# Performance work log

Measured on AMD Instinct MI355X. Metric: run time of the kernel, lower is better.

Reference implementation:

```python
import jax, jax.numpy as jnp
import numpy as np

NUM_GROUPS = 32
EPS = 1e-6


def setup_inputs() -> dict:
    key = jax.random.key(0)
    ks = jax.random.split(key, 10)
    B, C, L = 8, 512, 4096
    s = 1.0 / np.sqrt(C)
    x = jax.random.normal(ks[0], (B, C, L), dtype=jnp.float32)
    gn_w = jnp.ones((C,), jnp.float32)
    gn_b = jnp.zeros((C,), jnp.float32)
    wq = jax.random.normal(ks[1], (C, C), jnp.float32) * s
    bq = jax.random.normal(ks[2], (C,), jnp.float32) * 0.01
    wk = jax.random.normal(ks[3], (C, C), jnp.float32) * s
    bk = jax.random.normal(ks[4], (C,), jnp.float32) * 0.01
    wv = jax.random.normal(ks[5], (C, C), jnp.float32) * s
    bv = jax.random.normal(ks[6], (C,), jnp.float32) * 0.01
    wo = jax.random.normal(ks[7], (C, C), jnp.float32) * s
    bo = jax.random.normal(ks[8], (C,), jnp.float32) * 0.01
    return {"x": x, "gn_w": gn_w, "gn_b": gn_b, "wq": wq, "bq": bq,
            "wk": wk, "bk": bk, "wv": wv, "bv": bv, "wo": wo, "bo": bo}


def _group_norm(x, w, b):
    # x: [B, C, L]; normalize over each group's (C/G, L) slice
    B, C, L = x.shape
    g = x.reshape(B, NUM_GROUPS, C // NUM_GROUPS, L)
    mu = jnp.mean(g, axis=(2, 3), keepdims=True)
    var = jnp.var(g, axis=(2, 3), keepdims=True)
    g = (g - mu) * jax.lax.rsqrt(var + EPS)
    return g.reshape(B, C, L) * w[None, :, None] + b[None, :, None]


def _conv1x1(h, w, b):
    # pointwise conv: [B,C,L] x [Cout,Cin] -> [B,Cout,L]
    return jnp.einsum('oc,bcl->bol', w, h) + b[None, :, None]


def reference(x, gn_w, gn_b, wq, bq, wk, bk, wv, bv, wo, bo):
    h = _group_norm(x, gn_w, gn_b)
    q = _conv1x1(h, wq, bq)
    k = _conv1x1(h, wk, bk)
    v = _conv1x1(h, wv, bv)
    B, C, L = q.shape
    scale = jnp.asarray(C, q.dtype) ** -0.5
    # w_[b,i,j] = sum_c q[b,c,i] k[b,c,j]
    w_ = jnp.einsum('bci,bcj->bij', q, k) * scale
    w_ = jax.nn.softmax(w_, axis=2)
    # h[b,c,i] = sum_j v[b,c,j] w_[b,i,j]
    h = jnp.einsum('bcj,bij->bci', v, w_)
    return x + _conv1x1(h, wo, bo)
```

## Files before the change

kernel.cpp:

```cpp
#include <hip/hip_runtime.h>
#include <hip/hip_bf16.h>
#include <math.h>

#define DI __device__ __forceinline__

typedef unsigned short u16;
typedef unsigned int   u32;
typedef unsigned long long u64;
typedef __attribute__((ext_vector_type(8))) short short8;
typedef __attribute__((ext_vector_type(4))) float f32x4;

constexpr int CB = 512;
constexpr int LL = 4096;
constexpr int NG = 32;
constexpr long NELC = (long)LL * CB;

DI float bf2f(u16 u) { u32 v = ((u32)u) << 16; float f; __builtin_memcpy(&f, &v, 4); return f; }
DI u16 f2bf(float f) {
  u32 u; __builtin_memcpy(&u, &f, 4);
  u += 0x7fffu + ((u >> 16) & 1u);
  return (u16)(u >> 16);
}

DI void gload16(const void* g, void* l) {
  __builtin_amdgcn_global_load_lds((const __attribute__((address_space(1))) u32*)g,
                                   (__attribute__((address_space(3))) u32*)l, 16, 0, 0);
}

__global__ __launch_bounds__(256) void prep(
    const float* __restrict__ wq, const float* __restrict__ wk,
    const float* __restrict__ wv, const float* __restrict__ wo,
    const float* __restrict__ bq, const float* __restrict__ bk,
    const float* __restrict__ bv, const float* __restrict__ x,
    u16* __restrict__ wqkv, u16* __restrict__ wob, float* __restrict__ bqkv,
    float* __restrict__ stats) {
  if (blockIdx.x < 1024) {
    int i = blockIdx.x * 256 + threadIdx.x;
    wqkv[i]          = f2bf(wq[i]);
    wqkv[262144 + i] = f2bf(wk[i]);
    wqkv[524288 + i] = f2bf(wv[i]);
    wob[i]           = f2bf(wo[i]);
  } else if (blockIdx.x == 1024) {
    for (int j = 0; j < 6; ++j) {
      int idx = j * 256 + threadIdx.x;
      float b = (idx < 512) ? bq[idx] : (idx < 1024) ? bk[idx - 512] : bv[idx - 1024];
      bqkv[idx] = b;
    }
  } else {
    const int bid = blockIdx.x - 1025;
    const float4* base = (const float4*)(x + (long)bid * (16 * LL));
    float s = 0.f, ss = 0.f;
    for (int i = threadIdx.x; i < 16 * LL / 4; i += 256) {
      float4 v = base[i];
      s  += v.x + v.y + v.z + v.w;
      ss += v.x * v.x + v.y * v.y + v.z * v.z + v.w * v.w;
    }
#pragma unroll
    for (int o = 32; o; o >>= 1) { s += __shfl_xor(s, o); ss += __shfl_xor(ss, o); }
    __shared__ float red[8];
    int wv2 = threadIdx.x >> 6, ln = threadIdx.x & 63;
    if (ln == 0) { red[wv2 * 2] = s; red[wv2 * 2 + 1] = ss; }
    __syncthreads();
    if (threadIdx.x == 0) {
      float S = red[0] + red[2] + red[4] + red[6];
      float SS = red[1] + red[3] + red[5] + red[7];
      float mu = S * (1.f / 65536.f);
      float var = SS * (1.f / 65536.f) - mu * mu;
      stats[bid * 2]     = mu;
      stats[bid * 2 + 1] = rsqrtf(var + 1e-6f);
    }
  }
}

__global__ __launch_bounds__(256) void gn_apply(
    const float* __restrict__ x, const float* __restrict__ gw,
    const float* __restrict__ gb, const float* __restrict__ stats,
    u16* __restrict__ hT) {
  __shared__ u16 t[64][66];
  const int b = blockIdx.z, c0 = blockIdx.y * 64, l0 = blockIdx.x * 64;
  const int tid = threadIdx.x;
#pragma unroll
  for (int p = 0; p < 4; ++p) {
    const int cr = p * 16 + (tid >> 4);
    const int lq = (tid & 15) * 4;
    const int c = c0 + cr;
    const float mu = stats[(b * NG + (c >> 4)) * 2];
    const float rs = stats[(b * NG + (c >> 4)) * 2 + 1];
    const float g = gw[c], be = gb[c];
    float4 v = *(const float4*)(x + (long)b * CB * LL + (long)c * LL + l0 + lq);
    t[cr][lq + 0] = f2bf((v.x - mu) * rs * g + be);
    t[cr][lq + 1] = f2bf((v.y - mu) * rs * g + be);
    t[cr][lq + 2] = f2bf((v.z - mu) * rs * g + be);
    t[cr][lq + 3] = f2bf((v.w - mu) * rs * g + be);
  }
  __syncthreads();
#pragma unroll
  for (int it = 0; it < 2; ++it) {
    const int i = it * 2048 + tid * 8;
    const int lr = i >> 6, cc = i & 63;
    short8 val;
#pragma unroll
    for (int j = 0; j < 8; ++j) val[j] = (short)t[cc + j][lr];
    *(short8*)(hT + (long)b * LL * CB + (long)(l0 + lr) * CB + c0 + cc) = val;
  }
}

template <int Q>
DI void rdA(const u16* LB, int wr, int fr, int fq, short8 af[2][2]) {
#pragma unroll
  for (int m2 = 0; m2 < 2; ++m2)
#pragma unroll
    for (int kk = 0; kk < 2; ++kk) {
      const int R = wr * 128 + (Q * 2 + m2) * 16 + fr;
      af[m2][kk] = *(const short8*)((const char*)LB + R * 128 +
                                    ((kk * 64 + fq * 16) ^ ((R & 7) << 4)));
    }
}
DI void rdB(const u16* LB, int wc, int fr, int fq, short8 bf[4][2]) {
#pragma unroll
  for (int nf = 0; nf < 4; ++nf)
#pragma unroll
    for (int kk = 0; kk < 2; ++kk) {
      const int R = wc * 64 + nf * 16 + fr;
      bf[nf][kk] = *(const short8*)((const char*)LB + R * 128 +
                                    ((kk * 64 + fq * 16) ^ ((R & 7) << 4)));
    }
}
template <int Q>
DI void mmaQ(short8 af[2][2], short8 bf[4][2], f32x4 acc[8][4]) {
#pragma unroll
  for (int kk = 0; kk < 2; ++kk)
#pragma unroll
    for (int m2 = 0; m2 < 2; ++m2)
#pragma unroll
      for (int nf = 0; nf < 4; ++nf)
        acc[Q * 2 + m2][nf] = __builtin_amdgcn_mfma_f32_16x16x32_bf16(
            af[m2][kk], bf[nf][kk], acc[Q * 2 + m2][nf], 0, 0, 0);
}

#define PTAIL(Q)                                             \
  __builtin_amdgcn_s_barrier();                              \
  asm volatile("s_waitcnt lgkmcnt(0)" ::: "memory");         \
  __builtin_amdgcn_sched_barrier(0);                         \
  __builtin_amdgcn_s_setprio(1);                             \
  mmaQ<Q>(af, bf, acc);                                      \
  __builtin_amdgcn_s_setprio(0);                             \
  __builtin_amdgcn_s_barrier();

template <int EPI>
__global__ __launch_bounds__(512, 2) void gemm8p(
    const u16* __restrict__ A, int lda, long asb,
    const u16* __restrict__ Bt, int ldb, long bsb,
    int K, const float* __restrict__ bias, float scale,
    u16* __restrict__ o0, u16* __restrict__ o1, u16* __restrict__ o2,
    const float* __restrict__ rls, float* __restrict__ spp,
    long osb, int ldo) {
  __shared__ u16 smem[65536];
  u16* lA0 = smem;
  u16* lA1 = smem + 16384;
  u16* lB0 = smem + 32768;
  u16* lB1 = smem + 49152;

  const int tid = threadIdx.x;
  const int lane = tid & 63, wv = tid >> 6;
  const int wr = wv >> 2, wc = wv & 3;
  const int fr = lane & 15, fq = lane >> 4;
  const int bx = blockIdx.x, by = blockIdx.y, bz = blockIdx.z;
  const int bzb = (EPI == 2) ? (bz >> 2) : bz;
  const int tb  = (EPI == 2) ? (bz & 3) * (K >> 6) : 0;

  const u16* Ab = A + (long)bzb * asb + (long)(by * 256) * lda;
  const u16* Bb = Bt + (long)bzb * bsb + (long)(bx * 256) * ldb;

  auto stage = [&](u16* lbase, const u16* gbase, int ld_, int half, int t) {
#pragma unroll
    for (int p = 0; p < 2; ++p) {
      int i = p * 512 + tid;
      int row = i >> 3, ch = i & 7;
      int src = t * 64 + ((((ch << 4) ^ ((row & 7) << 4))) >> 1);
      gload16(gbase + (long)(half * 128 + row) * ld_ + src,
              lbase + half * 8192 + i * 8);
    }
  };

  f32x4 acc[8][4];
#pragma unroll
  for (int m = 0; m < 8; ++m)
#pragma unroll
    for (int n = 0; n < 4; ++n) acc[m][n] = (f32x4)(0.f);

  stage(lA0, Ab, lda, 0, tb); stage(lA0, Ab, lda, 1, tb);
  stage(lB0, Bb, ldb, 0, tb); stage(lB0, Bb, ldb, 1, tb);
  stage(lB1, Bb, ldb, 0, tb + 1); stage(lB1, Bb, ldb, 1, tb + 1);
  asm volatile("s_waitcnt vmcnt(4)" ::: "memory");
  __builtin_amdgcn_sched_barrier(0);
  __builtin_amdgcn_s_barrier();

  const int nt = K >> 6;
  short8 af[2][2], bf[4][2];
  for (int i = 0; i < nt / 2; ++i) {
    const bool last = (i == nt / 2 - 1);
    const int t1 = tb + 2 * i + 1, t2 = tb + 2 * i + 2, t3 = tb + 2 * i + 3;
    rdB(lB0, wc, fr, fq, bf);
    rdA<0>(lA0, wr, fr, fq, af);
    stage(lA1, Ab, lda, 0, t1);
    PTAIL(0)
    rdA<1>(lA0, wr, fr, fq, af);
    stage(lA1, Ab, lda, 1, t1);
    PTAIL(1)
    rdA<2>(lA0, wr, fr, fq, af);
    if (!last) stage(lB0, Bb, ldb, 0, t2);
    PTAIL(2)
    rdA<3>(lA0, wr, fr, fq, af);
    if (!last) stage(lB0, Bb, ldb, 1, t2);
    if (last) { asm volatile("s_waitcnt vmcnt(0)" ::: "memory"); }
    else      { asm volatile("s_waitcnt vmcnt(4)" ::: "memory"); }
    __builtin_amdgcn_sched_barrier(0);
    PTAIL(3)
    rdB(lB1, wc, fr, fq, bf);
    rdA<0>(lA1, wr, fr, fq, af);
    if (!last) stage(lA0, Ab, lda, 0, t2);
    PTAIL(0)
    rdA<1>(lA1, wr, fr, fq, af);
    if (!last) stage(lA0, Ab, lda, 1, t2);
    PTAIL(1)
    rdA<2>(lA1, wr, fr, fq, af);
    if (!last) stage(lB1, Bb, ldb, 0, t3);
    PTAIL(2)
    rdA<3>(lA1, wr, fr, fq, af);
    if (!last) stage(lB1, Bb, ldb, 1, t3);
    if (!last) {
      asm volatile("s_waitcnt vmcnt(4)" ::: "memory");
      __builtin_amdgcn_sched_barrier(0);
    }
    PTAIL(3)
  }

  if constexpr (EPI == 1) {
#pragma unroll
    for (int mf = 0; mf < 8; ++mf)
#pragma unroll
      for (int nf = 0; nf < 4; ++nf) {
        const int nl = wc * 64 + nf * 16 + fr;
#pragma unroll
        for (int r = 0; r < 4; ++r) {
          const int ml = wr * 128 + mf * 16 + fq * 4 + r;
          smem[ml * 256 + (nl ^ ((ml & 7) << 3))] =
              f2bf(exp2f(acc[mf][nf][r] * scale));
        }
      }
    __syncthreads();
    u16* dst0 = o0 + (long)bz * osb + (long)(by * 256) * ldo + bx * 256;
    float* sppb = spp + ((long)bz * 16 + bx) * LL + by * 256;
    for (int i = tid * 8; i < 65536; i += 4096) {
      const int rr = i >> 8, cc = i & 255;
      short8 val = *(const short8*)&smem[rr * 256 + (cc ^ ((rr & 7) << 3))];
      *(short8*)(dst0 + (long)rr * ldo + cc) = val;
      float s = 0.f;
#pragma unroll
      for (int j = 0; j < 8; ++j) s += bf2f((u16)val[j]);
      s += __shfl_xor(s, 1);  s += __shfl_xor(s, 2);
      s += __shfl_xor(s, 4);  s += __shfl_xor(s, 8);
      s += __shfl_xor(s, 16);
      if ((tid & 31) == 0) sppb[rr] = s;
    }
  } else if constexpr (EPI == 2) {
    const float* rl = rls + (long)bzb * LL + by * 256;
#pragma unroll
    for (int mf = 0; mf < 8; ++mf)
#pragma unroll
      for (int nf = 0; nf < 4; ++nf) {
        const int nl = wc * 64 + nf * 16 + fr;
#pragma unroll
        for (int r = 0; r < 4; ++r) {
          const int ml = wr * 128 + mf * 16 + fq * 4 + r;
          smem[ml * 256 + (nl ^ ((ml & 7) << 3))] =
              f2bf(acc[mf][nf][r] * rl[ml]);
        }
      }
    __syncthreads();
    u16* dst0 = o0 + (long)bzb * 4 * NELC + (long)(by * 256) * 2048 +
                (bz & 3) * 512 + bx * 256;
    for (int i = tid * 8; i < 65536; i += 4096) {
      const int rr = i >> 8, cc = i & 255;
      short8 val = *(const short8*)&smem[rr * 256 + (cc ^ ((rr & 7) << 3))];
      *(short8*)(dst0 + (long)rr * 2048 + cc) = val;
    }
  } else {
    const int mat = by >> 1;
    if (mat < 2) {
#pragma unroll
      for (int mf = 0; mf < 8; ++mf)
#pragma unroll
        for (int nf = 0; nf < 4; ++nf) {
          const int nl = wc * 64 + nf * 16 + fr;
#pragma unroll
          for (int r = 0; r < 4; ++r) {
            const int ml = wr * 128 + mf * 16 + fq * 4 + r;
            smem[nl * 256 + (ml ^ ((nl & 7) << 3))] =
                f2bf(acc[mf][nf][r] + bias[by * 256 + ml]);
          }
        }
      __syncthreads();
      u16* dst0 = (mat == 0 ? o0 : o1) + (long)bz * NELC +
                  (long)(bx * 256) * CB + ((by * 256) & 511);
      for (int i = tid * 8; i < 65536; i += 4096) {
        const int rr = i >> 8, cc = i & 255;
        short8 val = *(const short8*)&smem[rr * 256 + (cc ^ ((rr & 7) << 3))];
        *(short8*)(dst0 + (long)rr * CB + cc) = val;
      }
    } else {
#pragma unroll
      for (int mf = 0; mf < 8; ++mf)
#pragma unroll
        for (int nf = 0; nf < 4; ++nf) {
          const int nl = wc * 64 + nf * 16 + fr;
#pragma unroll
          for (int r = 0; r < 4; ++r) {
            const int ml = wr * 128 + mf * 16 + fq * 4 + r;
            smem[ml * 256 + (nl ^ ((ml & 7) << 3))] =
                f2bf(acc[mf][nf][r] + bias[by * 256 + ml]);
          }
        }
      __syncthreads();
      u16* dst0 = o2 + (long)bz * ((long)CB * LL) +
                  (long)((by * 256) & 511) * LL + bx * 256;
      for (int i = tid * 8; i < 65536; i += 4096) {
        const int rr = i >> 8, cc = i & 255;
        short8 val = *(const short8*)&smem[rr * 256 + (cc ^ ((rr & 7) << 3))];
        *(short8*)(dst0 + (long)rr * LL + cc) = val;
      }
    }
  }
}

template <int BM, int BN, int EPI, bool SWZ, int WR, int WC>
__global__ __launch_bounds__(WR * WC * 64) void gemm_bt(
    const u16* __restrict__ A, int lda, long asb,
    const u16* __restrict__ Bt, int ldb, long bsb,
    int K, const float* __restrict__ bias, float scale,
    u16* __restrict__ o0, u16* __restrict__ o1, u16* __restrict__ o2,
    float* __restrict__ of, const float* __restrict__ xres, long osb, int ldo) {
  constexpr int NT = WR * WC * 64;
  constexpr int FM = BM / WR / 16, FN = BN / WC / 16;
  static_assert((BM * 8) % NT == 0 && (BN * 8) % NT == 0, "staging div");
  __shared__ u16 smem[(BM + BN) * 64];
  u16* lA = smem;
  u16* lB = smem + BM * 64;

  int bx = blockIdx.x, by = blockIdx.y;
  if constexpr (SWZ) {
    const int nwg = gridDim.x * gridDim.y;
    const int id = by * gridDim.x + bx;
    const int id2 = (id & 7) * (nwg >> 3) + (id >> 3);
    bx = id2 % gridDim.x;
    by = id2 / gridDim.x;
  }

  const int tid = threadIdx.x;
  const int lane = tid & 63;
  const int wv = tid >> 6;
  const int wr = wv / WC, wc = wv % WC;
  const int fr = lane & 15, fq = lane >> 4;
  const int bz = blockIdx.z;
  const int bzb  = (EPI == 4) ? (bz >> 1) : bz;
  const int kbeg = (EPI == 4) ? (bz & 1) * K : 0;

  const u16* Ab = A + (long)bzb * asb + (long)(by * BM) * lda;
  const u16* Bb = Bt + (long)bzb * bsb + (long)(bx * BN) * ldb;

  f32x4 acc[FM][FN];
#pragma unroll
  for (int m = 0; m < FM; ++m)
#pragma unroll
    for (int n = 0; n < FN; ++n) acc[m][n] = (f32x4)(0.f);

  for (int k0 = kbeg; k0 < kbeg + K; k0 += 64) {
#pragma unroll
    for (int p = 0; p < BM * 8 / NT; ++p) {
      int t = p * NT + tid;
      int row = t >> 3;
      int cbl = ((t & 7) << 4) ^ ((row & 7) << 4);
      gload16(Ab + (long)row * lda + k0 + (cbl >> 1), &lA[t * 8]);
    }
#pragma unroll
    for (int p = 0; p < BN * 8 / NT; ++p) {
      int t = p * NT + tid;
      int row = t >> 3;
      int cbl = ((t & 7) << 4) ^ ((row & 7) << 4);
      gload16(Bb + (long)row * ldb + k0 + (cbl >> 1), &lB[t * 8]);
    }
    __syncthreads();
#pragma unroll
    for (int ks = 0; ks < 2; ++ks) {
      short8 af[FM], bfr[FN];
#pragma unroll
      for (int m = 0; m < FM; ++m) {
        int row = wr * (BM / WR) + m * 16 + fr;
        int cb = (ks * 64 + fq * 16) ^ ((row & 7) << 4);
        af[m] = *(const short8*)((const char*)lA + row * 128 + cb);
      }
#pragma unroll
      for (int n = 0; n < FN; ++n) {
        int row = wc * (BN / WC) + n * 16 + fr;
        int cb = (ks * 64 + fq * 16) ^ ((row & 7) << 4);
        bfr[n] = *(const short8*)((const char*)lB + row * 128 + cb);
      }
#pragma unroll
      for (int m = 0; m < FM; ++m)
#pragma unroll
        for (int n = 0; n < FN; ++n)
          acc[m][n] = __builtin_amdgcn_mfma_f32_16x16x32_bf16(af[m], bfr[n], acc[m][n], 0, 0, 0);
    }
    __syncthreads();
  }

  const int ml0 = wr * (BM / WR);
  const int nl0 = wc * (BN / WC);

  if constexpr (EPI == 3) {
    const int mg0 = by * BM + ml0;
    const int ng0 = bx * BN + nl0;
#pragma unroll
    for (int m = 0; m < FM; ++m)
#pragma unroll
      for (int n = 0; n < FN; ++n) {
        const int ng = ng0 + n * 16 + fr;
#pragma unroll
        for (int r = 0; r < 4; ++r) {
          const int mg = mg0 + m * 16 + fq * 4 + r;
          const long off = (long)bz * osb + (long)mg * ldo + ng;
          of[off] = acc[m][n][r] + bias[mg] + xres[off];
        }
      }
  } else {
    const float* rls = xres + (long)(bz >> 1) * LL + by * BM;
#pragma unroll
    for (int m = 0; m < FM; ++m)
#pragma unroll
      for (int n = 0; n < FN; ++n) {
        const int nl = nl0 + n * 16 + fr;
#pragma unroll
        for (int r = 0; r < 4; ++r) {
          const int ml = ml0 + m * 16 + fq * 4 + r;
          smem[ml * BN + (nl ^ ((ml & 7) << 3))] = f2bf(acc[m][n][r] * rls[ml]);
        }
      }
    __syncthreads();
    u16* dst0 = ((bz & 1) ? o1 : o0) + (long)(bz >> 1) * NELC +
                (long)(by * BM) * ldo + bx * BN;
    for (int i = tid * 8; i < BM * BN; i += NT * 8) {
      const int rr = i / BN, cc = i % BN;
      short8 val = *(const short8*)&smem[rr * BN + (cc ^ ((rr & 7) << 3))];
      *(short8*)(dst0 + (long)rr * ldo + cc) = val;
    }
  }
}

__global__ __launch_bounds__(256) void rls_combine(const float* __restrict__ spp,
                                                   float* __restrict__ rls) {
  const int row = blockIdx.x * 256 + threadIdx.x;
  const int z = blockIdx.y;
  const float* b = spp + (long)z * 16 * LL + row;
  float s = 0.f;
#pragma unroll
  for (int j = 0; j < 16; ++j) s += b[(long)j * LL];
  rls[(long)z * LL + row] = 1.0f / s;
}

__global__ __launch_bounds__(256) void reduce4(
    const u16* __restrict__ P, u16* __restrict__ o) {
  const int b = blockIdx.y;
  const long idx = (long)blockIdx.x * 256 + threadIdx.x;
  const int i = (int)(idx >> 6);
  const int c0 = ((int)idx & 63) * 8;
  const u16* Pb = P + (long)b * 4 * NELC + (long)i * 2048;
  float s[8] = {0.f, 0.f, 0.f, 0.f, 0.f, 0.f, 0.f, 0.f};
#pragma unroll
  for (int c4 = 0; c4 < 4; ++c4) {
    short8 v = *(const short8*)(Pb + c4 * 512 + c0);
#pragma unroll
    for (int j = 0; j < 8; ++j) s[j] += bf2f((u16)v[j]);
  }
  short8 r;
#pragma unroll
  for (int j = 0; j < 8; ++j) r[j] = (short)f2bf(s[j]);
  *(short8*)(o + (long)b * NELC + (long)i * 512 + c0) = r;
}

__global__ __launch_bounds__(256) void reduce_pp(
    const u16* __restrict__ p0, const u16* __restrict__ p1, u16* __restrict__ o) {
  const long base = (long)blockIdx.y * NELC +
                    (long)(blockIdx.x * 256 + threadIdx.x) * 16;
#pragma unroll
  for (int h = 0; h < 2; ++h) {
    short8 a = *(const short8*)(p0 + base + h * 8);
    short8 b = *(const short8*)(p1 + base + h * 8);
    short8 r;
#pragma unroll
    for (int j = 0; j < 8; ++j)
      r[j] = (short)f2bf(bf2f((u16)a[j]) + bf2f((u16)b[j]));
    *(short8*)(o + base + h * 8) = r;
  }
}

extern "C" void kernel_launch(void* const* d_in, const int* in_sizes, int n_in,
                              void* d_out, int out_size, void* d_ws, size_t ws_size,
                              hipStream_t stream) {
  const float* x   = (const float*)d_in[0];
  const float* gnw = (const float*)d_in[1];
  const float* gnb = (const float*)d_in[2];
  const float* wq  = (const float*)d_in[3];
  const float* bq  = (const float*)d_in[4];
  const float* wk  = (const float*)d_in[5];
  const float* bk  = (const float*)d_in[6];
  const float* wv  = (const float*)d_in[7];
  const float* bv  = (const float*)d_in[8];
  const float* wo  = (const float*)d_in[9];
  const float* bo  = (const float*)d_in[10];
  float* out = (float*)d_out;

  char* ws = (char*)d_ws;
  const long NEL = NELC;
  const long SEL = (long)LL * LL;
  float* stats = (float*)ws;
  float* bqkv  = (float*)(ws + 8192);
  u16* wqkv = (u16*)(ws + 16384);
  u16* wob  = (u16*)(ws + 16384 + 1572864);
  float* spp  = (float*)(ws + 2113536);
  float* rlsm = (float*)(ws + (3l << 20));
  u16* hT   = (u16*)(ws + (4l << 20));
  u16* qT   = hT + 8 * NEL;
  u16* kT   = qT + 8 * NEL;
  u16* vN   = kT + 8 * NEL;
  const size_t base = (4ul << 20) + 4ul * 8 * NEL * 2;

  const int G = (ws_size >= base + 2ul * SEL * 2) ? 2 : 1;
  u16* Sbuf = (G == 2) ? (u16*)(ws + base) : hT;

  prep<<<1281, 256, 0, stream>>>(wq, wk, wv, wo, bq, bk, bv, x,
                                 wqkv, wob, bqkv, stats);
  gn_apply<<<dim3(64, 8, 8), 256, 0, stream>>>(x, gnw, gnb, stats, hT);

  gemm8p<0><<<dim3(16, 6, 8), 512, 0, stream>>>(
      wqkv, 512, 0, hT, 512, NEL, 512, bqkv, 1.f, qT, kT, vN,
      nullptr, nullptr, 0, 0);

  const float cl = (1.0f / sqrtf(512.0f)) * 1.44269504f;
  for (int g0 = 0; g0 < 8; g0 += G) {
    gemm8p<1><<<dim3(16, 16, G), 512, 0, stream>>>(
        qT + (long)g0 * NEL, 512, NEL, kT + (long)g0 * NEL, 512, NEL, 512,
        nullptr, cl, Sbuf, nullptr, nullptr, nullptr, spp, SEL, LL);
    rls_combine<<<dim3(16, G), 256, 0, stream>>>(spp, rlsm);
    if (G == 2) {
      gemm8p<2><<<dim3(2, 16, 8), 512, 0, stream>>>(
          Sbuf, LL, SEL, vN + (long)g0 * NEL, LL, NEL, 1024,
          nullptr, 1.f, hT, nullptr, nullptr, rlsm, nullptr, 0, 0);
      reduce4<<<dim3(1024, 2), 256, 0, stream>>>(hT, qT + (long)g0 * NEL);
    } else {
      gemm_bt<128, 128, 4, true, 2, 4><<<dim3(4, 32, 2), 512, 0, stream>>>(
          Sbuf, LL, SEL, vN + (long)g0 * NEL, LL, NEL, 2048,
          nullptr, 1.f, qT + (long)g0 * NEL, kT + (long)g0 * NEL, nullptr,
          nullptr, rlsm, 0, CB);
      reduce_pp<<<dim3(512, 1), 256, 0, stream>>>(
          qT + (long)g0 * NEL, kT + (long)g0 * NEL, qT + (long)g0 * NEL);
    }
  }

  gemm_bt<128, 128, 3, false, 2, 2><<<dim3(32, 4, 8), 256, 0, stream>>>(
      wob, 512, 0, qT, 512, NEL, 512, bo, 1.f,
      nullptr, nullptr, nullptr, out, x, NEL, LL);

  (void)in_sizes; (void)n_in; (void)out_size; (void)ws_size;
}
```

Measured before the change: 566.9 us.

## Use 128x512 tile kernel for PV GEMM and fold row-sum reciprocal into epilogue

Replaces the 256x256-tile split-K P·V GEMM with a dedicated kernel that tiles 128 rows by the full 512 channels, so each block reads its slice of the score matrix once instead of twice across column blocks. The per-row softmax denominators are now summed and inverted inside this kernel's epilogue from the partial sums, which removes the separate rls_combine launch on the G==2 path. The trade-off is a larger LDS footprint (160KB) and a different register split per wave, which may affect occupancy and LDS staging balance.

```diff
diff --git a/kernel.cpp b/kernel.cpp
--- a/kernel.cpp
+++ b/kernel.cpp
@@ -153,8 +153,7 @@
     const u16* __restrict__ Bt, int ldb, long bsb,
     int K, const float* __restrict__ bias, float scale,
     u16* __restrict__ o0, u16* __restrict__ o1, u16* __restrict__ o2,
-    const float* __restrict__ rls, float* __restrict__ spp,
-    long osb, int ldo) {
+    float* __restrict__ spp, long osb, int ldo) {
   __shared__ u16 smem[65536];
   u16* lA0 = smem;
   u16* lA1 = smem + 16384;
@@ -166,11 +165,9 @@
   const int wr = wv >> 2, wc = wv & 3;
   const int fr = lane & 15, fq = lane >> 4;
   const int bx = blockIdx.x, by = blockIdx.y, bz = blockIdx.z;
-  const int bzb = (EPI == 2) ? (bz >> 2) : bz;
-  const int tb  = (EPI == 2) ? (bz & 3) * (K >> 6) : 0;
-
-  const u16* Ab = A + (long)bzb * asb + (long)(by * 256) * lda;
-  const u16* Bb = Bt + (long)bzb * bsb + (long)(bx * 256) * ldb;
+
+  const u16* Ab = A + (long)bz * asb + (long)(by * 256) * lda;
+  const u16* Bb = Bt + (long)bz * bsb + (long)(bx * 256) * ldb;
 
   auto stage = [&](u16* lbase, const u16* gbase, int ld_, int half, int t) {
 #pragma unroll
@@ -189,9 +186,9 @@
 #pragma unroll
     for (int n = 0; n < 4; ++n) acc[m][n] = (f32x4)(0.f);
 
-  stage(lA0, Ab, lda, 0, tb); stage(lA0, Ab, lda, 1, tb);
-  stage(lB0, Bb, ldb, 0, tb); stage(lB0, Bb, ldb, 1, tb);
-  stage(lB1, Bb, ldb, 0, tb + 1); stage(lB1, Bb, ldb, 1, tb + 1);
+  stage(lA0, Ab, lda, 0, 0); stage(lA0, Ab, lda, 1, 0);
+  stage(lB0, Bb, ldb, 0, 0); stage(lB0, Bb, ldb, 1, 0);
+  stage(lB1, Bb, ldb, 0, 1); stage(lB1, Bb, ldb, 1, 1);
   asm volatile("s_waitcnt vmcnt(4)" ::: "memory");
   __builtin_amdgcn_sched_barrier(0);
   __builtin_amdgcn_s_barrier();
@@ -200,7 +197,7 @@
   short8 af[2][2], bf[4][2];
   for (int i = 0; i < nt / 2; ++i) {
     const bool last = (i == nt / 2 - 1);
-    const int t1 = tb + 2 * i + 1, t2 = tb + 2 * i + 2, t3 = tb + 2 * i + 3;
+    const int t1 = 2 * i + 1, t2 = 2 * i + 2, t3 = 2 * i + 3;
     rdB(lB0, wc, fr, fq, bf);
     rdA<0>(lA0, wr, fr, fq, af);
     stage(lA1, Ab, lda, 0, t1);
@@ -264,28 +261,6 @@
       s += __shfl_xor(s, 16);
       if ((tid & 31) == 0) sppb[rr] = s;
     }
-  } else if constexpr (EPI == 2) {
-    const float* rl = rls + (long)bzb * LL + by * 256;
-#pragma unroll
-    for (int mf = 0; mf < 8; ++mf)
-#pragma unroll
-      for (int nf = 0; nf < 4; ++nf) {
-        const int nl = wc * 64 + nf * 16 + fr;
-#pragma unroll
-        for (int r = 0; r < 4; ++r) {
-          const int ml = wr * 128 + mf * 16 + fq * 4 + r;
-          smem[ml * 256 + (nl ^ ((ml & 7) << 3))] =
-              f2bf(acc[mf][nf][r] * rl[ml]);
-        }
-      }
-    __syncthreads();
-    u16* dst0 = o0 + (long)bzb * 4 * NELC + (long)(by * 256) * 2048 +
-                (bz & 3) * 512 + bx * 256;
-    for (int i = tid * 8; i < 65536; i += 4096) {
-      const int rr = i >> 8, cc = i & 255;
-      short8 val = *(const short8*)&smem[rr * 256 + (cc ^ ((rr & 7) << 3))];
-      *(short8*)(dst0 + (long)rr * 2048 + cc) = val;
-    }
   } else {
     const int mat = by >> 1;
     if (mat < 2) {
@@ -334,6 +309,171 @@
   }
 }
 
+DI void rdAall(const u16* LB, int wr, int fr, int fq, short8 af[4][2]) {
+#pragma unroll
+  for (int mf = 0; mf < 4; ++mf)
+#pragma unroll
+    for (int kk = 0; kk < 2; ++kk) {
+      const int R = wr * 64 + mf * 16 + fr;
+      af[mf][kk] = *(const short8*)((const char*)LB + R * 128 +
+                                    ((kk * 64 + fq * 16) ^ ((R & 7) << 4)));
+    }
+}
+template <int Q>
+DI void rdB2(const u16* LB, int wc, int fr, int fq, short8 bq[2][2]) {
+#pragma unroll
+  for (int n2 = 0; n2 < 2; ++n2)
+#pragma unroll
+    for (int kk = 0; kk < 2; ++kk) {
+      const int R = wc * 128 + (Q * 2 + n2) * 16 + fr;
+      bq[n2][kk] = *(const short8*)((const char*)LB + R * 128 +
+                                    ((kk * 64 + fq * 16) ^ ((R & 7) << 4)));
+    }
+}
+template <int Q>
+DI void mmaQ2(short8 af[4][2], short8 bq[2][2], f32x4 acc[4][8]) {
+#pragma unroll
+  for (int kk = 0; kk < 2; ++kk)
+#pragma unroll
+    for (int mf = 0; mf < 4; ++mf)
+#pragma unroll
+      for (int n2 = 0; n2 < 2; ++n2)
+        acc[mf][Q * 2 + n2] = __builtin_amdgcn_mfma_f32_16x16x32_bf16(
+            af[mf][kk], bq[n2][kk], acc[mf][Q * 2 + n2], 0, 0, 0);
+}
+
+#define PTAILW(Q)                                            \
+  __builtin_amdgcn_s_barrier();                              \
+  asm volatile("s_waitcnt lgkmcnt(0)" ::: "memory");         \
+  __builtin_amdgcn_sched_barrier(0);                         \
+  __builtin_amdgcn_s_setprio(1);                             \
+  mmaQ2<Q>(af, bq, acc);                                     \
+  __builtin_amdgcn_s_setprio(0);                             \
+  __builtin_amdgcn_s_barrier();
+
+__global__ __launch_bounds__(512, 2) void gemm8pw(
+    const u16* __restrict__ A, int lda, long asb,
+    const u16* __restrict__ Bt, int ldb, long bsb,
+    int K, u16* __restrict__ o0, const float* __restrict__ spp, int ldo) {
+  __shared__ u16 smem[81920];
+  u16* lA0 = smem;
+  u16* lA1 = smem + 8192;
+  u16* lB0 = smem + 16384;
+  u16* lB1 = smem + 49152;
+
+  const int tid = threadIdx.x;
+  const int lane = tid & 63, wv = tid >> 6;
+  const int wr = wv >> 2, wc = wv & 3;
+  const int fr = lane & 15, fq = lane >> 4;
+  const int by = blockIdx.x;
+  const int bz = blockIdx.z;
+  const int bzb = bz >> 2;
+  const int tb = (bz & 3) * (K >> 6);
+
+  const u16* Ab = A + (long)bzb * asb + (long)(by * 128) * lda;
+  const u16* Bb = Bt + (long)bzb * bsb;
+
+  auto stageA = [&](u16* lbase, int half, int t) {
+    int row = tid >> 3, ch = tid & 7;
+    int src = t * 64 + ((((ch << 4) ^ ((row & 7) << 4))) >> 1);
+    gload16(Ab + (long)(half * 64 + row) * lda + src,
+            lbase + half * 4096 + tid * 8);
+  };
+  auto stageB = [&](u16* lbase, int half, int t) {
+#pragma unroll
+    for (int p = 0; p < 4; ++p) {
+      int i = p * 512 + tid;
+      int row = i >> 3, ch = i & 7;
+      int src = t * 64 + ((((ch << 4) ^ ((row & 7) << 4))) >> 1);
+      gload16(Bb + (long)(half * 256 + row) * ldb + src,
+              lbase + half * 16384 + i * 8);
+    }
+  };
+
+  f32x4 acc[4][8];
+#pragma unroll
+  for (int m = 0; m < 4; ++m)
+#pragma unroll
+    for (int n = 0; n < 8; ++n) acc[m][n] = (f32x4)(0.f);
+
+  stageA(lA0, 0, tb); stageA(lA0, 1, tb);
+  stageB(lB0, 0, tb); stageB(lB0, 1, tb);
+  stageA(lA1, 0, tb + 1); stageA(lA1, 1, tb + 1);
+  asm volatile("s_waitcnt vmcnt(2)" ::: "memory");
+  __builtin_amdgcn_sched_barrier(0);
+  __builtin_amdgcn_s_barrier();
+
+  const int nt = K >> 6;
+  short8 af[4][2], bq[2][2];
+  for (int i = 0; i < nt / 2; ++i) {
+    const bool last = (i == nt / 2 - 1);
+    const int t1 = tb + 2 * i + 1, t2 = tb + 2 * i + 2, t3 = tb + 2 * i + 3;
+    rdAall(lA0, wr, fr, fq, af);
+    rdB2<0>(lB0, wc, fr, fq, bq);
+    stageB(lB1, 0, t1);
+    PTAILW(0)
+    rdB2<1>(lB0, wc, fr, fq, bq);
+    stageB(lB1, 1, t1);
+    PTAILW(1)
+    rdB2<2>(lB0, wc, fr, fq, bq);
+    if (!last) stageA(lA0, 0, t2);
+    PTAILW(2)
+    rdB2<3>(lB0, wc, fr, fq, bq);
+    if (!last) stageA(lA0, 1, t2);
+    if (last) { asm volatile("s_waitcnt vmcnt(0)" ::: "memory"); }
+    else      { asm volatile("s_waitcnt vmcnt(2)" ::: "memory"); }
+    __builtin_amdgcn_sched_barrier(0);
+    PTAILW(3)
+    rdAall(lA1, wr, fr, fq, af);
+    rdB2<0>(lB1, wc, fr, fq, bq);
+    if (!last) stageB(lB0, 0, t2);
+    PTAILW(0)
+    rdB2<1>(lB1, wc, fr, fq, bq);
+    if (!last) stageB(lB0, 1, t2);
+    PTAILW(1)
+    rdB2<2>(lB1, wc, fr, fq, bq);
+    if (!last) stageA(lA1, 0, t3);
+    PTAILW(2)
+    rdB2<3>(lB1, wc, fr, fq, bq);
+    if (!last) stageA(lA1, 1, t3);
+    if (!last) {
+      asm volatile("s_waitcnt vmcnt(2)" ::: "memory");
+      __builtin_amdgcn_sched_barrier(0);
+    }
+    PTAILW(3)
+  }
+
+  float* rlb = (float*)(smem + 73728);
+  if (tid < 128) {
+    const float* sp = spp + (long)bzb * 16 * LL + by * 128 + tid;
+    float s = 0.f;
+#pragma unroll
+    for (int j = 0; j < 16; ++j) s += sp[(long)j * LL];
+    rlb[tid] = 1.0f / s;
+  }
+  __syncthreads();
+
+#pragma unroll
+  for (int mf = 0; mf < 4; ++mf)
+#pragma unroll
+    for (int nf = 0; nf < 8; ++nf) {
+      const int nl = wc * 128 + nf * 16 + fr;
+#pragma unroll
+      for (int r = 0; r < 4; ++r) {
+        const int ml = wr * 64 + mf * 16 + fq * 4 + r;
+        smem[ml * 512 + (nl ^ ((ml & 7) << 3))] =
+            f2bf(acc[mf][nf][r] * rlb[ml]);
+      }
+    }
+  __syncthreads();
+  u16* dst0 = o0 + (long)bzb * 4 * NELC + (long)(by * 128) * ldo + (bz & 3) * 512;
+  for (int i = tid * 8; i < 65536; i += 4096) {
+    const int rr = i >> 9, cc = i & 511;
+    short8 val = *(const short8*)&smem[rr * 512 + (cc ^ ((rr & 7) << 3))];
+    *(short8*)(dst0 + (long)rr * ldo + cc) = val;
+  }
+}
+
 template <int BM, int BN, int EPI, bool SWZ, int WR, int WC>
 __global__ __launch_bounds__(WR * WC * 64) void gemm_bt(
     const u16* __restrict__ A, int lda, long asb,
@@ -544,20 +684,19 @@
 
   gemm8p<0><<<dim3(16, 6, 8), 512, 0, stream>>>(
       wqkv, 512, 0, hT, 512, NEL, 512, bqkv, 1.f, qT, kT, vN,
-      nullptr, nullptr, 0, 0);
+      nullptr, 0, 0);
 
   const float cl = (1.0f / sqrtf(512.0f)) * 1.44269504f;
   for (int g0 = 0; g0 < 8; g0 += G) {
     gemm8p<1><<<dim3(16, 16, G), 512, 0, stream>>>(
         qT + (long)g0 * NEL, 512, NEL, kT + (long)g0 * NEL, 512, NEL, 512,
-        nullptr, cl, Sbuf, nullptr, nullptr, nullptr, spp, SEL, LL);
-    rls_combine<<<dim3(16, G), 256, 0, stream>>>(spp, rlsm);
+        nullptr, cl, Sbuf, nullptr, nullptr, spp, SEL, LL);
     if (G == 2) {
-      gemm8p<2><<<dim3(2, 16, 8), 512, 0, stream>>>(
-          Sbuf, LL, SEL, vN + (long)g0 * NEL, LL, NEL, 1024,
-          nullptr, 1.f, hT, nullptr, nullptr, rlsm, nullptr, 0, 0);
+      gemm8pw<<<dim3(32, 1, 8), 512, 0, stream>>>(
+          Sbuf, LL, SEL, vN + (long)g0 * NEL, LL, NEL, 1024, hT, spp, 2048);
       reduce4<<<dim3(1024, 2), 256, 0, stream>>>(hT, qT + (long)g0 * NEL);
     } else {
+      rls_combine<<<dim3(16, 1), 256, 0, stream>>>(spp, rlsm);
       gemm_bt<128, 128, 4, true, 2, 4><<<dim3(4, 32, 2), 512, 0, stream>>>(
           Sbuf, LL, SEL, vN + (long)g0 * NEL, LL, NEL, 2048,
           nullptr, 1.f, qT + (long)g0 * NEL, kT + (long)g0 * NEL, nullptr,
```

New measurement: 577.7 us. About the same (+1.9%).
